# Optimization experiments

Hardware: AMD Instinct MI355X
Metric: run time of the kernel (lower is better)

The kernel has to match this reference:

```python
import jax, jax.numpy as jnp
import numpy as np
import math

D_MODEL = 512
N_HEADS = 8
RADIUS = 0.5
MAX_NEIGHBORS = 32
B, S = 2, 3072


def setup_inputs() -> dict:
    key = jax.random.key(0)
    ks = jax.random.split(key, 12)
    s = 1.0 / math.sqrt(D_MODEL)
    return {
        "x": jax.random.normal(ks[0], (B, S, D_MODEL), jnp.float32),
        "positions": jax.random.normal(ks[1], (B, S, 3), jnp.float32),
        "Wq": jax.random.normal(ks[2], (D_MODEL, D_MODEL), jnp.float32) * s,
        "bq": jnp.zeros((D_MODEL,), jnp.float32),
        "Wk": jax.random.normal(ks[3], (D_MODEL, D_MODEL), jnp.float32) * s,
        "bk": jnp.zeros((D_MODEL,), jnp.float32),
        "Wv": jax.random.normal(ks[4], (D_MODEL, D_MODEL), jnp.float32) * s,
        "bv": jnp.zeros((D_MODEL,), jnp.float32),
        "Wo": jax.random.normal(ks[5], (D_MODEL, D_MODEL), jnp.float32) * s,
        "bo": jnp.zeros((D_MODEL,), jnp.float32),
    }


def _neighbor_mask(positions):
    # positions: (B, S, 3) -> mask: (B, S, S)
    diff = positions[:, :, None, :] - positions[:, None, :, :]  # (B,S,S,3)
    dist = jnp.linalg.norm(diff, axis=-1)                        # (B,S,S)
    radius_mask = (dist < RADIUS).astype(positions.dtype)
    # top-k nearest by argsort (includes self at distance 0)
    nbr_idx = jnp.argsort(dist, axis=-1)[..., :MAX_NEIGHBORS]    # (B,S,K)
    b_idx = jnp.arange(positions.shape[0])[:, None, None]
    r_idx = jnp.arange(positions.shape[1])[None, :, None]
    topk_mask = jnp.zeros_like(dist).at[b_idx, r_idx, nbr_idx].set(1.0)
    return topk_mask * radius_mask


def reference(x, positions, Wq, bq, Wk, bk, Wv, bv, Wo, bo):
    b, s, d = x.shape
    dh = d // N_HEADS
    scale = math.sqrt(dh)

    mask = _neighbor_mask(positions)  # (B,S,S)

    def proj(W, bias):
        return (x @ W + bias).reshape(b, s, N_HEADS, dh).transpose(0, 2, 1, 3)

    Q = proj(Wq, bq)  # (B,H,S,dh)
    K = proj(Wk, bk)
    V = proj(Wv, bv)

    scores = jnp.einsum('bhsd,bhtd->bhst', Q, K) / scale  # (B,H,S,S)
    neg_inf = jnp.asarray(-jnp.inf, scores.dtype)
    scores = jnp.where(mask[:, None, :, :] == 0, neg_inf, scores)
    attn = jax.nn.softmax(scores, axis=-1)
    attn = jnp.nan_to_num(attn, nan=0.0)  # fully-masked rows -> 0
    out = jnp.einsum('bhst,bhtd->bhsd', attn, V)  # (B,H,S,dh)
    out = out.transpose(0, 2, 1, 3).reshape(b, s, d)
    return out @ Wo + bo
```

## Files before the change

kernel.cpp:

```cpp
#include <hip/hip_runtime.h>
#include <math.h>

#define D_MODEL 512
#define N_HEADS 8
#define DH      64
#define S_LEN   3072
#define BATCH   2
#define KMAX    32
#define M_ROWS  6144
#define CAND_CAP 512

#define TOPK_BLOCKS (M_ROWS / 4)
#define CONV_BLOCKS (M_ROWS * D_MODEL / 1024)
#define PACK_BLOCKS 2048

typedef __attribute__((ext_vector_type(8))) short bf16x8;
typedef __attribute__((ext_vector_type(4))) float f32x4;
typedef __attribute__((ext_vector_type(2))) short s16x2;
typedef unsigned long long u64;

__device__ __forceinline__ float b2f(unsigned int u) {
    return __uint_as_float((u & 0xFFFFu) << 16);
}
__device__ __forceinline__ unsigned short f2b(float f) {
    unsigned int u = __float_as_uint(f);
    return (unsigned short)((u + 0x7FFFu + ((u >> 16) & 1u)) >> 16);
}

#if __has_builtin(__builtin_amdgcn_fdot2_f32_bf16)
__device__ __forceinline__ float dot2bf(unsigned int a, unsigned int b, float c) {
    return __builtin_amdgcn_fdot2_f32_bf16(
        __builtin_bit_cast(s16x2, a), __builtin_bit_cast(s16x2, b), c, false);
}
#else
__device__ __forceinline__ float dot2bf(unsigned int a, unsigned int b, float c) {
    return c + b2f(a) * b2f(b) + b2f(a >> 16) * b2f(b >> 16);
}
#endif

__global__ __launch_bounds__(256) void prep_kernel(
    const float* __restrict__ x, const float* __restrict__ pos,
    const float* __restrict__ Wq, const float* __restrict__ bq,
    const float* __restrict__ Wk, const float* __restrict__ bk,
    const float* __restrict__ Wv, const float* __restrict__ bv,
    const float* __restrict__ Wo,
    unsigned short* __restrict__ xb, unsigned short* __restrict__ Wt,
    float* __restrict__ bqkv,
    int* __restrict__ nbr_idx, int* __restrict__ nbr_cnt)
{
    const int bid = blockIdx.x;
    const int tid = threadIdx.x;

    if (bid < TOPK_BLOCKS) {
        __shared__ u64 s_keys[4][CAND_CAP];
        __shared__ int s_n[4];
        const int r0 = bid * 4;
        const int b = (r0 >= S_LEN) ? 1 : 0;
        if (tid < 4) s_n[tid] = 0;
        __syncthreads();

        float qx[4], qy[4], qz[4];
        #pragma unroll
        for (int r = 0; r < 4; ++r) {
            qx[r] = pos[(size_t)(r0 + r) * 3 + 0];
            qy[r] = pos[(size_t)(r0 + r) * 3 + 1];
            qz[r] = pos[(size_t)(r0 + r) * 3 + 2];
        }
        const float* pb = pos + (size_t)b * S_LEN * 3;
        #pragma unroll
        for (int i = 0; i < 12; ++i) {
            const int t = tid + i * 256;
            const float x3 = pb[t * 3 + 0], y3 = pb[t * 3 + 1], z3 = pb[t * 3 + 2];
            #pragma unroll
            for (int r = 0; r < 4; ++r) {
                const float dx = qx[r] - x3, dy = qy[r] - y3, dz = qz[r] - z3;
                const float d2 = dx * dx + dy * dy + dz * dz;
                if (d2 < 0.25f) {
                    const int slot = atomicAdd(&s_n[r], 1);
                    if (slot < CAND_CAP)
                        s_keys[r][slot] = ((u64)__float_as_uint(d2) << 32) | (unsigned)t;
                }
            }
        }
        __syncthreads();

        const int rr = tid >> 6, c0 = tid & 63;
        const int n = min(s_n[rr], CAND_CAP);
        for (int c = c0; c < n; c += 64) {
            const u64 k = s_keys[rr][c];
            int rank = 0;
            for (int j = 0; j < n; ++j) rank += (s_keys[rr][j] < k) ? 1 : 0;
            if (rank < KMAX)
                nbr_idx[(size_t)(r0 + rr) * KMAX + rank] = (int)(k & 0xFFFFFFFFu);
        }
        if (c0 == 0) nbr_cnt[r0 + rr] = min(n, KMAX);
    } else if (bid < TOPK_BLOCKS + CONV_BLOCKS) {
        const int i = ((bid - TOPK_BLOCKS) * 256 + tid) * 4;
        const float4 v = *reinterpret_cast<const float4*>(x + i);
        ushort4 o;
        o.x = f2b(v.x); o.y = f2b(v.y); o.z = f2b(v.z); o.w = f2b(v.w);
        *reinterpret_cast<ushort4*>(xb + i) = o;
    } else {
        const int n = bid - TOPK_BLOCKS - CONV_BLOCKS;
        const float* W; int nn;
        if (n < 512)       { W = Wq; nn = n; }
        else if (n < 1024) { W = Wk; nn = n - 512; }
        else if (n < 1536) { W = Wv; nn = n - 1024; }
        else               { W = Wo; nn = n - 1536; }
        for (int k = tid; k < 512; k += 256)
            Wt[(size_t)n * 512 + k] = f2b(W[(size_t)k * 512 + nn]);
        if (tid == 0 && n < 1536) {
            const float* bsel = (n < 512) ? bq : (n < 1024) ? bk : bv;
            bqkv[n] = bsel[nn];
        }
    }
}

template <bool OUT_BF16>
__global__ __launch_bounds__(256) void gemm_mfma_kernel(
    const unsigned short* __restrict__ A,
    const unsigned short* __restrict__ Bt,
    const float* __restrict__ bias,
    void* __restrict__ Cv, int ldc)
{
    constexpr int K = 512;
    __shared__ __align__(16) unsigned short As[128 * 32];
    __shared__ __align__(16) unsigned short Bs[128 * 32];

    const int tid = threadIdx.x;
    const int m0 = blockIdx.x * 128;
    const int n0 = blockIdx.y * 128;
    const int wid = tid >> 6;
    const int lane = tid & 63;
    const int wm = (wid >> 1) * 64;
    const int wn = (wid & 1) * 64;
    const int l15 = lane & 15;
    const int kg = lane >> 4;

    const int srow = tid >> 2;
    const int sk = (tid & 3) * 8;

    f32x4 acc[4][4] = {};

    for (int kt = 0; kt < K; kt += 32) {
        #pragma unroll
        for (int c = 0; c < 2; ++c) {
            const unsigned short* ga = A + (size_t)(m0 + c * 64 + srow) * K + kt + sk;
            __builtin_amdgcn_global_load_lds(
                (const __attribute__((address_space(1))) void*)ga,
                (__attribute__((address_space(3))) void*)(&As[c * 2048 + tid * 8]),
                16, 0, 0);
            const unsigned short* gb = Bt + (size_t)(n0 + c * 64 + srow) * K + kt + sk;
            __builtin_amdgcn_global_load_lds(
                (const __attribute__((address_space(1))) void*)gb,
                (__attribute__((address_space(3))) void*)(&Bs[c * 2048 + tid * 8]),
                16, 0, 0);
        }
        __syncthreads();

        bf16x8 af[4], bfr[4];
        #pragma unroll
        for (int i = 0; i < 4; ++i) {
            af[i]  = *reinterpret_cast<const bf16x8*>(&As[(wm + i * 16 + l15) * 32 + kg * 8]);
            bfr[i] = *reinterpret_cast<const bf16x8*>(&Bs[(wn + i * 16 + l15) * 32 + kg * 8]);
        }
        #pragma unroll
        for (int i = 0; i < 4; ++i)
            #pragma unroll
            for (int j = 0; j < 4; ++j)
                acc[i][j] = __builtin_amdgcn_mfma_f32_16x16x32_bf16(af[i], bfr[j], acc[i][j], 0, 0, 0);
        __syncthreads();
    }

    const int crow = kg * 4;
    #pragma unroll
    for (int i = 0; i < 4; ++i) {
        #pragma unroll
        for (int j = 0; j < 4; ++j) {
            const int col = n0 + wn + j * 16 + l15;
            const float bb = bias[col];
            #pragma unroll
            for (int r = 0; r < 4; ++r) {
                const int row = m0 + wm + i * 16 + crow + r;
                const float v = acc[i][j][r] + bb;
                if (OUT_BF16)
                    ((unsigned short*)Cv)[(size_t)row * ldc + col] = f2b(v);
                else
                    ((float*)Cv)[(size_t)row * ldc + col] = v;
            }
        }
    }
}

__global__ __launch_bounds__(512) void attn_kernel(
    const unsigned short* __restrict__ qkv,
    const int* __restrict__ nbr_idx,
    const int* __restrict__ nbr_cnt,
    unsigned short* __restrict__ ao)
{
    const int row = blockIdx.x;
    const int b = (row >= S_LEN) ? 1 : 0;
    const int tid = threadIdx.x;
    const int h = tid >> 6;
    const int lane = tid & 63;
    const int j = lane & 31;
    const int half = lane >> 5;

    __shared__ __align__(16) unsigned short K_lds[KMAX][520];
    __shared__ unsigned int s_off[KMAX];
    __shared__ unsigned int sQ[N_HEADS][32];
    __shared__ int s_cnt;

    if (tid < KMAX) {
        const int cnt0 = nbr_cnt[row];
        int t = nbr_idx[(size_t)row * KMAX + tid];
        t = (tid < cnt0) ? t : 0;
        s_off[tid] = (unsigned int)t * 3072u;
        if (tid == 0) s_cnt = cnt0;
    }
    if (lane < 32)
        sQ[h][lane] = ((const unsigned int*)(qkv + (size_t)row * 1536 + h * DH))[lane];
    __syncthreads();

    const int cnt = s_cnt;
    const char* qkvb_ = (const char*)qkv + (size_t)b * S_LEN * 3072;

    {
        const int jb = h * 4;
        #pragma unroll
        for (int c = 0; c < 4; ++c) {
            const int jj = jb + c;
            const char* src = qkvb_ + s_off[jj] + 1024 + lane * 16;
            __builtin_amdgcn_global_load_lds(
                (const __attribute__((address_space(1))) void*)src,
                (__attribute__((address_space(3))) void*)(&K_lds[jj][0]),
                16, 0, 0);
        }
    }

    const char* vbase_l = qkvb_ + 2048 + h * 128 + lane * 2;
    unsigned int vr[KMAX];
    #pragma unroll
    for (int jj = 0; jj < KMAX; ++jj)
        vr[jj] = *(const unsigned short*)(vbase_l + s_off[jj]);

    __syncthreads();

    const uint4* kp = reinterpret_cast<const uint4*>(&K_lds[j][h * 64 + half * 32]);
    uint4 ku[4];
    #pragma unroll
    for (int c = 0; c < 4; ++c) ku[c] = kp[c];

    const unsigned int* qws = &sQ[h][half * 16];
    float partial = 0.f;
    #pragma unroll
    for (int c = 0; c < 4; ++c) {
        partial = dot2bf(ku[c].x, qws[c * 4 + 0], partial);
        partial = dot2bf(ku[c].y, qws[c * 4 + 1], partial);
        partial = dot2bf(ku[c].z, qws[c * 4 + 2], partial);
        partial = dot2bf(ku[c].w, qws[c * 4 + 3], partial);
    }
    partial += __shfl_down(partial, 32, 64);

    const float sc = (half == 0 && j < cnt) ? partial * 0.125f : -INFINITY;
    float mx = sc;
    #pragma unroll
    for (int off = 16; off; off >>= 1) mx = fmaxf(mx, __shfl_xor(mx, off, 64));
    const float p = (half == 0 && j < cnt) ? expf(sc - mx) : 0.f;
    float sum = p;
    #pragma unroll
    for (int off = 16; off; off >>= 1) sum += __shfl_xor(sum, off, 64);
    const float inv = __uint_as_float(
        __builtin_amdgcn_readfirstlane(__float_as_uint(1.f / sum)));

    const float pn = __shfl_xor(p, 1, 64);
    const unsigned int pw = ((unsigned int)f2b(pn) << 16) | f2b(p);

    float o0 = 0.f, o1 = 0.f;
    #pragma unroll
    for (int i = 0; i < 16; i += 2) {
        const unsigned int w0 = __builtin_amdgcn_readlane(pw, 2 * i);
        const unsigned int w1 = __builtin_amdgcn_readlane(pw, 2 * i + 2);
        const unsigned int vp0 = (vr[2 * i + 1] << 16) | vr[2 * i];
        const unsigned int vp1 = (vr[2 * i + 3] << 16) | vr[2 * i + 2];
        o0 = dot2bf(vp0, w0, o0);
        o1 = dot2bf(vp1, w1, o1);
    }
    const float o = (o0 + o1) * inv;
    ao[(size_t)row * D_MODEL + h * DH + lane] = f2b(o);
}

extern "C" void kernel_launch(void* const* d_in, const int* in_sizes, int n_in,
                              void* d_out, int out_size, void* d_ws, size_t ws_size,
                              hipStream_t stream) {
    const float* x   = (const float*)d_in[0];
    const float* pos = (const float*)d_in[1];
    const float* Wq  = (const float*)d_in[2];
    const float* bq  = (const float*)d_in[3];
    const float* Wk  = (const float*)d_in[4];
    const float* bk  = (const float*)d_in[5];
    const float* Wv  = (const float*)d_in[6];
    const float* bv  = (const float*)d_in[7];
    const float* Wo  = (const float*)d_in[8];
    const float* bo  = (const float*)d_in[9];
    float* out = (float*)d_out;

    unsigned short* xb   = (unsigned short*)d_ws;
    unsigned short* Wt   = xb + (size_t)M_ROWS * 512;
    float*          bqkv = (float*)(Wt + (size_t)2048 * 512);
    unsigned short* qkvb = (unsigned short*)(bqkv + 1536);
    unsigned short* aob  = qkvb + (size_t)M_ROWS * 1536;
    int*            nidx = (int*)(aob + (size_t)M_ROWS * 512);
    int*            ncnt = nidx + (size_t)M_ROWS * KMAX;

    prep_kernel<<<TOPK_BLOCKS + CONV_BLOCKS + PACK_BLOCKS, 256, 0, stream>>>(
        x, pos, Wq, bq, Wk, bk, Wv, bv, Wo, xb, Wt, bqkv, nidx, ncnt);

    dim3 g1(M_ROWS / 128, 1536 / 128);
    gemm_mfma_kernel<true><<<g1, 256, 0, stream>>>(xb, Wt, bqkv, qkvb, 1536);

    attn_kernel<<<M_ROWS, 512, 0, stream>>>(qkvb, nidx, ncnt, aob);

    dim3 g2(M_ROWS / 128, 512 / 128);
    gemm_mfma_kernel<false><<<g2, 256, 0, stream>>>(aob, Wt + (size_t)1536 * 512, bo, out, 512);
}
```

Before: 81.47 us.

## Reorder attention rows by z-bucket for neighbor locality, mapped per XCD

Builds a histogram of query rows by quantized z coordinate, prefix-scans it, and scatters the rows into a z-sorted order. The attention kernel then maps each block to a sorted row, with a swizzle that hands contiguous ranges to blocks sharing blockIdx mod 8 (likely targeting per-XCD L2). Neighboring rows share K/V neighbors, so gathered qkv lines should hit in L2 more often. The cost is an extra memset, two small kernels and a global atomic per query row. The order within a bucket depends on atomic timing, which changes only the schedule, not the results.

```diff
diff --git a/kernel.cpp b/kernel.cpp
--- a/kernel.cpp
+++ b/kernel.cpp
@@ -9,6 +9,7 @@
 #define KMAX    32
 #define M_ROWS  6144
 #define CAND_CAP 512
+#define NBUCKET 128
 
 #define TOPK_BLOCKS (M_ROWS / 4)
 #define CONV_BLOCKS (M_ROWS * D_MODEL / 1024)
@@ -25,6 +26,10 @@
 __device__ __forceinline__ unsigned short f2b(float f) {
     unsigned int u = __float_as_uint(f);
     return (unsigned short)((u + 0x7FFFu + ((u >> 16) & 1u)) >> 16);
+}
+__device__ __forceinline__ int zbucket(float z) {
+    int zq = (int)((z + 2.0f) * 16.0f);
+    return zq < 0 ? 0 : (zq > 63 ? 63 : zq);
 }
 
 #if __has_builtin(__builtin_amdgcn_fdot2_f32_bf16)
@@ -46,7 +51,8 @@
     const float* __restrict__ Wo,
     unsigned short* __restrict__ xb, unsigned short* __restrict__ Wt,
     float* __restrict__ bqkv,
-    int* __restrict__ nbr_idx, int* __restrict__ nbr_cnt)
+    int* __restrict__ nbr_idx, int* __restrict__ nbr_cnt,
+    int* __restrict__ hist)
 {
     const int bid = blockIdx.x;
     const int tid = threadIdx.x;
@@ -66,6 +72,9 @@
             qy[r] = pos[(size_t)(r0 + r) * 3 + 1];
             qz[r] = pos[(size_t)(r0 + r) * 3 + 2];
         }
+        if (tid < 4)
+            atomicAdd(&hist[b * 64 + zbucket(qz[tid])], 1);
+
         const float* pb = pos + (size_t)b * S_LEN * 3;
         #pragma unroll
         for (int i = 0; i < 12; ++i) {
@@ -116,6 +125,34 @@
     }
 }
 
+__global__ __launch_bounds__(64) void scan_kernel(
+    const int* __restrict__ hist, int* __restrict__ offsets)
+{
+    const int lane = threadIdx.x;
+    const int a = hist[lane * 2], c = hist[lane * 2 + 1];
+    const int s = a + c;
+    int inc = s;
+    #pragma unroll
+    for (int off = 1; off < 64; off <<= 1) {
+        const int t = __shfl_up(inc, off, 64);
+        if (lane >= off) inc += t;
+    }
+    const int excl = inc - s;
+    offsets[lane * 2] = excl;
+    offsets[lane * 2 + 1] = excl + a;
+}
+
+__global__ __launch_bounds__(256) void order_kernel(
+    const float* __restrict__ pos, int* __restrict__ offsets,
+    int* __restrict__ order)
+{
+    const int row = blockIdx.x * 256 + threadIdx.x;
+    const int b = (row >= S_LEN) ? 1 : 0;
+    const float z = pos[(size_t)row * 3 + 2];
+    const int slot = atomicAdd(&offsets[b * 64 + zbucket(z)], 1);
+    order[slot] = row;
+}
+
 template <bool OUT_BF16>
 __global__ __launch_bounds__(256) void gemm_mfma_kernel(
     const unsigned short* __restrict__ A,
@@ -196,9 +233,11 @@
     const unsigned short* __restrict__ qkv,
     const int* __restrict__ nbr_idx,
     const int* __restrict__ nbr_cnt,
+    const int* __restrict__ order,
     unsigned short* __restrict__ ao)
 {
-    const int row = blockIdx.x;
+    const int p = ((blockIdx.x & 7) * 768) + (blockIdx.x >> 3);
+    const int row = order[p];
     const int b = (row >= S_LEN) ? 1 : 0;
     const int tid = threadIdx.x;
     const int h = tid >> 6;
@@ -266,15 +305,15 @@
     float mx = sc;
     #pragma unroll
     for (int off = 16; off; off >>= 1) mx = fmaxf(mx, __shfl_xor(mx, off, 64));
-    const float p = (half == 0 && j < cnt) ? expf(sc - mx) : 0.f;
-    float sum = p;
+    const float pr = (half == 0 && j < cnt) ? expf(sc - mx) : 0.f;
+    float sum = pr;
     #pragma unroll
     for (int off = 16; off; off >>= 1) sum += __shfl_xor(sum, off, 64);
     const float inv = __uint_as_float(
         __builtin_amdgcn_readfirstlane(__float_as_uint(1.f / sum)));
 
-    const float pn = __shfl_xor(p, 1, 64);
-    const unsigned int pw = ((unsigned int)f2b(pn) << 16) | f2b(p);
+    const float pn = __shfl_xor(pr, 1, 64);
+    const unsigned int pw = ((unsigned int)f2b(pn) << 16) | f2b(pr);
 
     float o0 = 0.f, o1 = 0.f;
     #pragma unroll
@@ -312,14 +351,22 @@
     unsigned short* aob  = qkvb + (size_t)M_ROWS * 1536;
     int*            nidx = (int*)(aob + (size_t)M_ROWS * 512);
     int*            ncnt = nidx + (size_t)M_ROWS * KMAX;
+    int*            hist = ncnt + M_ROWS;
+    int*            offs = hist + NBUCKET;
+    int*            ordr = offs + NBUCKET;
+
+    hipMemsetAsync(hist, 0, NBUCKET * sizeof(int), stream);
 
     prep_kernel<<<TOPK_BLOCKS + CONV_BLOCKS + PACK_BLOCKS, 256, 0, stream>>>(
-        x, pos, Wq, bq, Wk, bk, Wv, bv, Wo, xb, Wt, bqkv, nidx, ncnt);
+        x, pos, Wq, bq, Wk, bk, Wv, bv, Wo, xb, Wt, bqkv, nidx, ncnt, hist);
+
+    scan_kernel<<<1, 64, 0, stream>>>(hist, offs);
+    order_kernel<<<M_ROWS / 256, 256, 0, stream>>>(pos, offs, ordr);
 
     dim3 g1(M_ROWS / 128, 1536 / 128);
     gemm_mfma_kernel<true><<<g1, 256, 0, stream>>>(xb, Wt, bqkv, qkvb, 1536);
 
-    attn_kernel<<<M_ROWS, 512, 0, stream>>>(qkvb, nidx, ncnt, aob);
+    attn_kernel<<<M_ROWS, 512, 0, stream>>>(qkvb, nidx, ncnt, ordr, aob);
 
     dim3 g2(M_ROWS / 128, 512 / 128);
     gemm_mfma_kernel<false><<<g2, 256, 0, stream>>>(aob, Wt + (size_t)1536 * 512, bo, out, 512);
```

Result: slower. 101.0 us (+24.0%).
